# Performance work log

Measured on AMD Instinct MI355X. Metric: run time of the kernel, lower is better.

Reference implementation:

```python
import jax, jax.numpy as jnp
import numpy as np

N_GROUPS = 4
N_LIMITED_GROUPS = 2
TOP_K = 2
ROUTE_SCALE = 1.0


def setup_inputs() -> dict:
    key = jax.random.key(0)
    k1, k2, k3, k4 = jax.random.split(key, 4)
    n_tokens, dim, n_experts = 65536, 4096, 16
    return {
        "x": jax.random.normal(k1, (n_tokens, dim), dtype=jnp.float32),
        "w1_weight": jax.random.normal(k2, (n_experts, dim), dtype=jnp.float32) * 0.02,
        "w1_bias": jax.random.normal(k3, (n_experts,), dtype=jnp.float32) * 0.02,
        "route_bias": jax.random.normal(k4, (n_experts,), dtype=jnp.float32) * 0.02,
    }


def reference(x, w1_weight, w1_bias, route_bias):
    # Linear scorer: [N, E]
    logits = x @ w1_weight.T + w1_bias
    # softmax in fp32 (score_func == 'softmax')
    scores = jax.nn.softmax(logits.astype(jnp.float32), axis=-1)
    # bias add (moe_use_bias=True); original_scores includes the bias
    scores = scores + route_bias
    original_scores = scores

    n = x.shape[0]
    # group masking: view [N, n_groups, experts_per_group]
    g = scores.reshape(n, N_GROUPS, -1)
    group_scores = g.max(axis=-1)  # amax path since bias is not None
    _, gidx = jax.lax.top_k(group_scores, N_LIMITED_GROUPS)  # [N, n_limited]
    keep = jnp.zeros((n, N_GROUPS), dtype=bool).at[
        jnp.arange(n)[:, None], gidx
    ].set(True)
    masked = jnp.where(keep[:, :, None], g, -jnp.inf).reshape(n, -1)

    # top-k over masked scores; gather values from original (unmasked-at-topk) scores
    _, indices = jax.lax.top_k(masked, TOP_K)  # [N, k]
    values = jnp.take_along_axis(original_scores, indices, axis=1) * ROUTE_SCALE
    return values.astype(x.dtype), indices
```

## Files before the change

### kernel.cpp

```cpp
#include <hip/hip_runtime.h>
#include <math.h>

constexpr int NE  = 16;
constexpr int NG  = 4;
constexpr int NSL = 4;
constexpr int KS  = 16;
constexpr int TPB = 128;
constexpr int LDS_BYTES = 52224;

__global__ __launch_bounds__(256)
void w_transpose_kernel(const float* __restrict__ w, float* __restrict__ wt,
                        int dim, int n) {
    int id = blockIdx.x * 256 + threadIdx.x;
    if (id < n) {
        int k = id / NE;
        int e = id - k * NE;
        wt[id] = w[(size_t)e * dim + k];
    }
}

template <int WT>
__global__ __launch_bounds__(256)
void router_kernel(const float* __restrict__ x,
                   const float* __restrict__ w1w,
                   const float* __restrict__ wt,
                   const float* __restrict__ w1b,
                   const float* __restrict__ rbias,
                   float* __restrict__ dout,
                   int n_tokens, int dim)
{
    __shared__ char ldsraw[LDS_BYTES];
    auto wbuf = (double (*)[KS][NE])ldsraw;

    const int tid  = threadIdx.x;
    const int uwid = __builtin_amdgcn_readfirstlane(tid >> 6);
    const int lane = tid & 63;
    const int slice = dim / NSL;
    const int nst  = slice / KS;
    const long tokA = (long)blockIdx.x * TPB + lane;
    const long tokB = tokA + 64;

    const float* xA = x + tokA * (size_t)dim + (size_t)uwid * slice;
    const float* xB = x + tokB * (size_t)dim + (size_t)uwid * slice;

    double accA[NE], accB[NE];
#pragma unroll
    for (int e = 0; e < NE; ++e) { accA[e] = 0.0; accB[e] = 0.0; }

    float4 a0 = *(const float4*)(xA + 0),  a1 = *(const float4*)(xA + 4);
    float4 a2 = *(const float4*)(xA + 8),  a3 = *(const float4*)(xA + 12);
    float4 b0 = *(const float4*)(xB + 0),  b1 = *(const float4*)(xB + 4);
    float4 b2 = *(const float4*)(xB + 8),  b3 = *(const float4*)(xB + 12);

    float4 wreg;
    if (WT) {
        wreg = *(const float4*)(wt + (size_t)uwid * slice * NE + lane * 4);
    } else {
        const int i0 = lane * 4;
#pragma unroll
        for (int j = 0; j < 4; ++j) {
            int i = i0 + j;
            ((float*)&wreg)[j] = w1w[(size_t)(i & 15) * dim + uwid * slice + (i >> 4)];
        }
    }

    for (int c = 0; c < nst; ++c) {
        {
            double* dst = &wbuf[uwid][0][0] + lane * 4;
            dst[0] = (double)wreg.x;  dst[1] = (double)wreg.y;
            dst[2] = (double)wreg.z;  dst[3] = (double)wreg.w;
        }

        float4 na0 = a0, na1 = a1, na2 = a2, na3 = a3;
        float4 nb0 = b0, nb1 = b1, nb2 = b2, nb3 = b3;
        if (c + 1 < nst) {
            const float* pa = xA + (c + 1) * KS;
            const float* pb = xB + (c + 1) * KS;
            na0 = *(const float4*)(pa + 0);  na1 = *(const float4*)(pa + 4);
            na2 = *(const float4*)(pa + 8);  na3 = *(const float4*)(pa + 12);
            nb0 = *(const float4*)(pb + 0);  nb1 = *(const float4*)(pb + 4);
            nb2 = *(const float4*)(pb + 8);  nb3 = *(const float4*)(pb + 12);
            if (WT) {
                wreg = *(const float4*)(wt + (size_t)(uwid * slice + (c + 1) * KS) * NE
                                        + lane * 4);
            } else {
                const int kb = uwid * slice + (c + 1) * KS;
                const int i0 = lane * 4;
#pragma unroll
                for (int j = 0; j < 4; ++j) {
                    int i = i0 + j;
                    ((float*)&wreg)[j] = w1w[(size_t)(i & 15) * dim + kb + (i >> 4)];
                }
            }
        }

        float fa[KS], fb[KS];
        fa[0]=a0.x;  fa[1]=a0.y;  fa[2]=a0.z;  fa[3]=a0.w;
        fa[4]=a1.x;  fa[5]=a1.y;  fa[6]=a1.z;  fa[7]=a1.w;
        fa[8]=a2.x;  fa[9]=a2.y;  fa[10]=a2.z; fa[11]=a2.w;
        fa[12]=a3.x; fa[13]=a3.y; fa[14]=a3.z; fa[15]=a3.w;
        fb[0]=b0.x;  fb[1]=b0.y;  fb[2]=b0.z;  fb[3]=b0.w;
        fb[4]=b1.x;  fb[5]=b1.y;  fb[6]=b1.z;  fb[7]=b1.w;
        fb[8]=b2.x;  fb[9]=b2.y;  fb[10]=b2.z; fb[11]=b2.w;
        fb[12]=b3.x; fb[13]=b3.y; fb[14]=b3.z; fb[15]=b3.w;

#pragma unroll
        for (int kk = 0; kk < KS; ++kk) {
            double xa_ = (double)fa[kk];
            double xb_ = (double)fb[kk];
#pragma unroll
            for (int ep = 0; ep < NE / 2; ++ep) {
                double2 wv = *(const double2*)&wbuf[uwid][kk][ep * 2];
                accA[ep * 2 + 0] = fma(xa_, wv.x, accA[ep * 2 + 0]);
                accA[ep * 2 + 1] = fma(xa_, wv.y, accA[ep * 2 + 1]);
                accB[ep * 2 + 0] = fma(xb_, wv.x, accB[ep * 2 + 0]);
                accB[ep * 2 + 1] = fma(xb_, wv.y, accB[ep * 2 + 1]);
            }
        }

        a0=na0; a1=na1; a2=na2; a3=na3;
        b0=nb0; b1=nb1; b2=nb2; b3=nb3;
    }

    __syncthreads();
    auto red = (double (*)[2][64][NE + 1])ldsraw;
    if (uwid != 0) {
#pragma unroll
        for (int e = 0; e < NE; ++e) {
            red[uwid - 1][0][lane][e] = accA[e];
            red[uwid - 1][1][lane][e] = accB[e];
        }
    }
    __syncthreads();
    if (uwid != 0) return;

#pragma unroll
    for (int t = 0; t < 2; ++t) {
        double tot[NE];
#pragma unroll
        for (int e = 0; e < NE; ++e) {
            double a = (t == 0) ? accA[e] : accB[e];
            tot[e] = ((a + red[0][t][lane][e]) + red[1][t][lane][e])
                     + red[2][t][lane][e];
        }

        double logit[NE];
        double m = -INFINITY;
#pragma unroll
        for (int e = 0; e < NE; ++e) {
            logit[e] = tot[e] + (double)w1b[e];
            m = fmax(m, logit[e]);
        }
        double ssum = 0.0;
        double p[NE];
#pragma unroll
        for (int e = 0; e < NE; ++e) { p[e] = exp(logit[e] - m); ssum += p[e]; }
        double inv = 1.0 / ssum;
        double sc[NE];
#pragma unroll
        for (int e = 0; e < NE; ++e) sc[e] = p[e] * inv + (double)rbias[e];

        double gm[NG];
#pragma unroll
        for (int g = 0; g < NG; ++g) {
            double a = fmax(sc[g * 4 + 0], sc[g * 4 + 1]);
            double b = fmax(sc[g * 4 + 2], sc[g * 4 + 3]);
            gm[g] = fmax(a, b);
        }
        int g1 = 0;
#pragma unroll
        for (int g = 1; g < NG; ++g) if (gm[g] > gm[g1]) g1 = g;
        int g2 = (g1 == 0) ? 1 : 0;
#pragma unroll
        for (int g = 0; g < NG; ++g) if (g != g1 && gm[g] > gm[g2]) g2 = g;

        double v1 = -INFINITY; int i1 = 0;
#pragma unroll
        for (int e = 0; e < NE; ++e) {
            int g = e >> 2;
            bool keep = (g == g1) || (g == g2);
            if (keep && sc[e] > v1) { v1 = sc[e]; i1 = e; }
        }
        double v2 = -INFINITY; int i2 = 0;
#pragma unroll
        for (int e = 0; e < NE; ++e) {
            int g = e >> 2;
            bool keep = ((g == g1) || (g == g2)) && (e != i1);
            if (keep && sc[e] > v2) { v2 = sc[e]; i2 = e; }
        }

        long tok = (t == 0) ? tokA : tokB;
        float2 vv; vv.x = (float)v1; vv.y = (float)v2;
        *(float2*)(dout + tok * 2) = vv;
        float2 iv; iv.x = (float)i1; iv.y = (float)i2;
        *(float2*)(dout + (long)n_tokens * 2 + tok * 2) = iv;
    }
}

extern "C" void kernel_launch(void* const* d_in, const int* in_sizes, int n_in,
                              void* d_out, int out_size, void* d_ws, size_t ws_size,
                              hipStream_t stream)
{
    const float* x   = (const float*)d_in[0];
    const float* w1w = (const float*)d_in[1];
    const float* w1b = (const float*)d_in[2];
    const float* rb  = (const float*)d_in[3];
    float* out = (float*)d_out;

    const int ne       = in_sizes[2];
    const int dim      = in_sizes[1] / ne;
    const int n_tokens = in_sizes[0] / dim;

    const int nW = dim * ne;
    const bool useT = ws_size >= (size_t)nW * sizeof(float);

    dim3 grid(n_tokens / TPB), block(NSL * 64);
    if (useT) {
        float* wt = (float*)d_ws;
        hipLaunchKernelGGL(w_transpose_kernel, dim3((nW + 255) / 256), dim3(256),
                           0, stream, w1w, wt, dim, nW);
        hipLaunchKernelGGL((router_kernel<1>), grid, block, 0, stream,
                           x, w1w, (const float*)wt, w1b, rb, out, n_tokens, dim);
    } else {
        hipLaunchKernelGGL((router_kernel<0>), grid, block, 0, stream,
                           x, w1w, (const float*)nullptr, w1b, rb, out, n_tokens, dim);
    }
}
```

Baseline: 297.1 us.

## Split router into partial-sum kernel with 8 K-slices and separate finalize kernel

The fused router kernel is split into two kernels. The first computes fp64 partial dot products over 8 K-slices per 128-token block with a smaller LDS footprint, aiming for higher occupancy, and writes the partials to workspace. The second kernel reduces the partials and runs the softmax and top-k selection. This removes the in-block LDS reduction and barriers, but adds 64 MB of fp64 partial traffic to global memory and an extra kernel launch. If the workspace is too small, a fallback fused kernel runs instead.

```diff
diff --git a/kernel.cpp b/kernel.cpp
--- a/kernel.cpp
+++ b/kernel.cpp
@@ -3,10 +3,9 @@
 
 constexpr int NE  = 16;
 constexpr int NG  = 4;
-constexpr int NSL = 4;
-constexpr int KS  = 16;
-constexpr int TPB = 128;
-constexpr int LDS_BYTES = 52224;
+constexpr int NSL = 8;
+constexpr int KS  = 8;
+constexpr int TPB1 = 128;
 
 __global__ __launch_bounds__(256)
 void w_transpose_kernel(const float* __restrict__ w, float* __restrict__ wt,
@@ -19,90 +18,54 @@
     }
 }
 
-template <int WT>
-__global__ __launch_bounds__(256)
-void router_kernel(const float* __restrict__ x,
-                   const float* __restrict__ w1w,
-                   const float* __restrict__ wt,
-                   const float* __restrict__ w1b,
-                   const float* __restrict__ rbias,
-                   float* __restrict__ dout,
-                   int n_tokens, int dim)
+__global__ __launch_bounds__(512, 4)
+void k1_partials(const float* __restrict__ x,
+                 const float* __restrict__ wt,
+                 double* __restrict__ P,
+                 int n_tokens, int dim)
 {
-    __shared__ char ldsraw[LDS_BYTES];
-    auto wbuf = (double (*)[KS][NE])ldsraw;
+    __shared__ double wbuf[NSL][KS][NE];
 
     const int tid  = threadIdx.x;
     const int uwid = __builtin_amdgcn_readfirstlane(tid >> 6);
     const int lane = tid & 63;
     const int slice = dim / NSL;
     const int nst  = slice / KS;
-    const long tokA = (long)blockIdx.x * TPB + lane;
+    const long tokA = (long)blockIdx.x * TPB1 + lane;
     const long tokB = tokA + 64;
 
     const float* xA = x + tokA * (size_t)dim + (size_t)uwid * slice;
     const float* xB = x + tokB * (size_t)dim + (size_t)uwid * slice;
+    const float* wp = wt + (size_t)uwid * slice * NE;
 
     double accA[NE], accB[NE];
 #pragma unroll
     for (int e = 0; e < NE; ++e) { accA[e] = 0.0; accB[e] = 0.0; }
 
-    float4 a0 = *(const float4*)(xA + 0),  a1 = *(const float4*)(xA + 4);
-    float4 a2 = *(const float4*)(xA + 8),  a3 = *(const float4*)(xA + 12);
-    float4 b0 = *(const float4*)(xB + 0),  b1 = *(const float4*)(xB + 4);
-    float4 b2 = *(const float4*)(xB + 8),  b3 = *(const float4*)(xB + 12);
-
-    float4 wreg;
-    if (WT) {
-        wreg = *(const float4*)(wt + (size_t)uwid * slice * NE + lane * 4);
-    } else {
-        const int i0 = lane * 4;
-#pragma unroll
-        for (int j = 0; j < 4; ++j) {
-            int i = i0 + j;
-            ((float*)&wreg)[j] = w1w[(size_t)(i & 15) * dim + uwid * slice + (i >> 4)];
-        }
-    }
+    float4 a0 = *(const float4*)(xA + 0), a1 = *(const float4*)(xA + 4);
+    float4 b0 = *(const float4*)(xB + 0), b1 = *(const float4*)(xB + 4);
+    float2 wreg = *(const float2*)(wp + lane * 2);
 
     for (int c = 0; c < nst; ++c) {
         {
-            double* dst = &wbuf[uwid][0][0] + lane * 4;
+            double* dst = &wbuf[uwid][0][0] + lane * 2;
             dst[0] = (double)wreg.x;  dst[1] = (double)wreg.y;
-            dst[2] = (double)wreg.z;  dst[3] = (double)wreg.w;
-        }
-
-        float4 na0 = a0, na1 = a1, na2 = a2, na3 = a3;
-        float4 nb0 = b0, nb1 = b1, nb2 = b2, nb3 = b3;
+        }
+
+        float4 na0 = a0, na1 = a1, nb0 = b0, nb1 = b1;
         if (c + 1 < nst) {
             const float* pa = xA + (c + 1) * KS;
             const float* pb = xB + (c + 1) * KS;
             na0 = *(const float4*)(pa + 0);  na1 = *(const float4*)(pa + 4);
-            na2 = *(const float4*)(pa + 8);  na3 = *(const float4*)(pa + 12);
             nb0 = *(const float4*)(pb + 0);  nb1 = *(const float4*)(pb + 4);
-            nb2 = *(const float4*)(pb + 8);  nb3 = *(const float4*)(pb + 12);
-            if (WT) {
-                wreg = *(const float4*)(wt + (size_t)(uwid * slice + (c + 1) * KS) * NE
-                                        + lane * 4);
-            } else {
-                const int kb = uwid * slice + (c + 1) * KS;
-                const int i0 = lane * 4;
-#pragma unroll
-                for (int j = 0; j < 4; ++j) {
-                    int i = i0 + j;
-                    ((float*)&wreg)[j] = w1w[(size_t)(i & 15) * dim + kb + (i >> 4)];
-                }
-            }
+            wreg = *(const float2*)(wp + (size_t)(c + 1) * KS * NE + lane * 2);
         }
 
         float fa[KS], fb[KS];
-        fa[0]=a0.x;  fa[1]=a0.y;  fa[2]=a0.z;  fa[3]=a0.w;
-        fa[4]=a1.x;  fa[5]=a1.y;  fa[6]=a1.z;  fa[7]=a1.w;
-        fa[8]=a2.x;  fa[9]=a2.y;  fa[10]=a2.z; fa[11]=a2.w;
-        fa[12]=a3.x; fa[13]=a3.y; fa[14]=a3.z; fa[15]=a3.w;
-        fb[0]=b0.x;  fb[1]=b0.y;  fb[2]=b0.z;  fb[3]=b0.w;
-        fb[4]=b1.x;  fb[5]=b1.y;  fb[6]=b1.z;  fb[7]=b1.w;
-        fb[8]=b2.x;  fb[9]=b2.y;  fb[10]=b2.z; fb[11]=b2.w;
-        fb[12]=b3.x; fb[13]=b3.y; fb[14]=b3.z; fb[15]=b3.w;
+        fa[0]=a0.x; fa[1]=a0.y; fa[2]=a0.z; fa[3]=a0.w;
+        fa[4]=a1.x; fa[5]=a1.y; fa[6]=a1.z; fa[7]=a1.w;
+        fb[0]=b0.x; fb[1]=b0.y; fb[2]=b0.z; fb[3]=b0.w;
+        fb[4]=b1.x; fb[5]=b1.y; fb[6]=b1.z; fb[7]=b1.w;
 
 #pragma unroll
         for (int kk = 0; kk < KS; ++kk) {
@@ -118,12 +81,184 @@
             }
         }
 
+        a0 = na0; a1 = na1; b0 = nb0; b1 = nb1;
+    }
+
+    double* pA = P + ((size_t)uwid * n_tokens + tokA) * NE;
+    double* pB = P + ((size_t)uwid * n_tokens + tokB) * NE;
+#pragma unroll
+    for (int j = 0; j < NE / 2; ++j) {
+        double2 v; v.x = accA[2 * j]; v.y = accA[2 * j + 1];
+        *(double2*)(pA + 2 * j) = v;
+    }
+#pragma unroll
+    for (int j = 0; j < NE / 2; ++j) {
+        double2 v; v.x = accB[2 * j]; v.y = accB[2 * j + 1];
+        *(double2*)(pB + 2 * j) = v;
+    }
+}
+
+__global__ __launch_bounds__(256)
+void k2_finalize(const double* __restrict__ P,
+                 const float* __restrict__ w1b,
+                 const float* __restrict__ rbias,
+                 float* __restrict__ dout,
+                 int n_tokens)
+{
+    const long t = (long)blockIdx.x * 256 + threadIdx.x;
+    if (t >= n_tokens) return;
+
+    double tot[NE];
+#pragma unroll
+    for (int e = 0; e < NE; ++e) tot[e] = 0.0;
+    for (int s = 0; s < NSL; ++s) {
+        const double* ps = P + ((size_t)s * n_tokens + t) * NE;
+#pragma unroll
+        for (int j = 0; j < NE / 2; ++j) {
+            double2 v = *(const double2*)(ps + 2 * j);
+            tot[2 * j + 0] += v.x;
+            tot[2 * j + 1] += v.y;
+        }
+    }
+
+    double logit[NE];
+    double m = -INFINITY;
+#pragma unroll
+    for (int e = 0; e < NE; ++e) {
+        logit[e] = tot[e] + (double)w1b[e];
+        m = fmax(m, logit[e]);
+    }
+    double ssum = 0.0;
+    double p[NE];
+#pragma unroll
+    for (int e = 0; e < NE; ++e) { p[e] = exp(logit[e] - m); ssum += p[e]; }
+    double inv = 1.0 / ssum;
+    double sc[NE];
+#pragma unroll
+    for (int e = 0; e < NE; ++e) sc[e] = p[e] * inv + (double)rbias[e];
+
+    double gm[NG];
+#pragma unroll
+    for (int g = 0; g < NG; ++g) {
+        double a = fmax(sc[g * 4 + 0], sc[g * 4 + 1]);
+        double b = fmax(sc[g * 4 + 2], sc[g * 4 + 3]);
+        gm[g] = fmax(a, b);
+    }
+    int g1 = 0;
+#pragma unroll
+    for (int g = 1; g < NG; ++g) if (gm[g] > gm[g1]) g1 = g;
+    int g2 = (g1 == 0) ? 1 : 0;
+#pragma unroll
+    for (int g = 0; g < NG; ++g) if (g != g1 && gm[g] > gm[g2]) g2 = g;
+
+    double v1 = -INFINITY; int i1 = 0;
+#pragma unroll
+    for (int e = 0; e < NE; ++e) {
+        int g = e >> 2;
+        bool keep = (g == g1) || (g == g2);
+        if (keep && sc[e] > v1) { v1 = sc[e]; i1 = e; }
+    }
+    double v2 = -INFINITY; int i2 = 0;
+#pragma unroll
+    for (int e = 0; e < NE; ++e) {
+        int g = e >> 2;
+        bool keep = ((g == g1) || (g == g2)) && (e != i1);
+        if (keep && sc[e] > v2) { v2 = sc[e]; i2 = e; }
+    }
+
+    float2 vv; vv.x = (float)v1; vv.y = (float)v2;
+    *(float2*)(dout + t * 2) = vv;
+    float2 iv; iv.x = (float)i1; iv.y = (float)i2;
+    *(float2*)(dout + (long)n_tokens * 2 + t * 2) = iv;
+}
+
+__global__ __launch_bounds__(256)
+void router_fallback(const float* __restrict__ x,
+                     const float* __restrict__ w1w,
+                     const float* __restrict__ w1b,
+                     const float* __restrict__ rbias,
+                     float* __restrict__ dout,
+                     int n_tokens, int dim)
+{
+    __shared__ double wbuf4[4][16][NE];
+    const int tid  = threadIdx.x;
+    const int uwid = __builtin_amdgcn_readfirstlane(tid >> 6);
+    const int lane = tid & 63;
+    const int slice = dim / 4;
+    const int nst  = slice / 16;
+    const long tokA = (long)blockIdx.x * 128 + lane;
+    const long tokB = tokA + 64;
+    const float* xA = x + tokA * (size_t)dim + (size_t)uwid * slice;
+    const float* xB = x + tokB * (size_t)dim + (size_t)uwid * slice;
+
+    double accA[NE], accB[NE];
+#pragma unroll
+    for (int e = 0; e < NE; ++e) { accA[e] = 0.0; accB[e] = 0.0; }
+
+    float4 a0 = *(const float4*)(xA + 0), a1 = *(const float4*)(xA + 4);
+    float4 a2 = *(const float4*)(xA + 8), a3 = *(const float4*)(xA + 12);
+    float4 b0 = *(const float4*)(xB + 0), b1 = *(const float4*)(xB + 4);
+    float4 b2 = *(const float4*)(xB + 8), b3 = *(const float4*)(xB + 12);
+    float4 wreg;
+    {
+        const int i0 = lane * 4;
+#pragma unroll
+        for (int j = 0; j < 4; ++j) {
+            int i = i0 + j;
+            ((float*)&wreg)[j] = w1w[(size_t)(i & 15) * dim + uwid * slice + (i >> 4)];
+        }
+    }
+
+    for (int c = 0; c < nst; ++c) {
+        {
+            double* dst = &wbuf4[uwid][0][0] + lane * 4;
+            dst[0] = (double)wreg.x;  dst[1] = (double)wreg.y;
+            dst[2] = (double)wreg.z;  dst[3] = (double)wreg.w;
+        }
+        float4 na0=a0,na1=a1,na2=a2,na3=a3,nb0=b0,nb1=b1,nb2=b2,nb3=b3;
+        if (c + 1 < nst) {
+            const float* pa = xA + (c + 1) * 16;
+            const float* pb = xB + (c + 1) * 16;
+            na0 = *(const float4*)(pa + 0);  na1 = *(const float4*)(pa + 4);
+            na2 = *(const float4*)(pa + 8);  na3 = *(const float4*)(pa + 12);
+            nb0 = *(const float4*)(pb + 0);  nb1 = *(const float4*)(pb + 4);
+            nb2 = *(const float4*)(pb + 8);  nb3 = *(const float4*)(pb + 12);
+            const int kb = uwid * slice + (c + 1) * 16;
+            const int i0 = lane * 4;
+#pragma unroll
+            for (int j = 0; j < 4; ++j) {
+                int i = i0 + j;
+                ((float*)&wreg)[j] = w1w[(size_t)(i & 15) * dim + kb + (i >> 4)];
+            }
+        }
+        float fa[16], fb[16];
+        fa[0]=a0.x; fa[1]=a0.y; fa[2]=a0.z; fa[3]=a0.w;
+        fa[4]=a1.x; fa[5]=a1.y; fa[6]=a1.z; fa[7]=a1.w;
+        fa[8]=a2.x; fa[9]=a2.y; fa[10]=a2.z; fa[11]=a2.w;
+        fa[12]=a3.x; fa[13]=a3.y; fa[14]=a3.z; fa[15]=a3.w;
+        fb[0]=b0.x; fb[1]=b0.y; fb[2]=b0.z; fb[3]=b0.w;
+        fb[4]=b1.x; fb[5]=b1.y; fb[6]=b1.z; fb[7]=b1.w;
+        fb[8]=b2.x; fb[9]=b2.y; fb[10]=b2.z; fb[11]=b2.w;
+        fb[12]=b3.x; fb[13]=b3.y; fb[14]=b3.z; fb[15]=b3.w;
+#pragma unroll
+        for (int kk = 0; kk < 16; ++kk) {
+            double xa_ = (double)fa[kk];
+            double xb_ = (double)fb[kk];
+#pragma unroll
+            for (int ep = 0; ep < NE / 2; ++ep) {
+                double2 wv = *(const double2*)&wbuf4[uwid][kk][ep * 2];
+                accA[ep*2+0] = fma(xa_, wv.x, accA[ep*2+0]);
+                accA[ep*2+1] = fma(xa_, wv.y, accA[ep*2+1]);
+                accB[ep*2+0] = fma(xb_, wv.x, accB[ep*2+0]);
+                accB[ep*2+1] = fma(xb_, wv.y, accB[ep*2+1]);
+            }
+        }
         a0=na0; a1=na1; a2=na2; a3=na3;
         b0=nb0; b1=nb1; b2=nb2; b3=nb3;
     }
 
     __syncthreads();
-    auto red = (double (*)[2][64][NE + 1])ldsraw;
+    __shared__ double red[3][2][64][NE + 1];
     if (uwid != 0) {
 #pragma unroll
         for (int e = 0; e < NE; ++e) {
@@ -143,7 +278,6 @@
             tot[e] = ((a + red[0][t][lane][e]) + red[1][t][lane][e])
                      + red[2][t][lane][e];
         }
-
         double logit[NE];
         double m = -INFINITY;
 #pragma unroll
@@ -151,20 +285,17 @@
             logit[e] = tot[e] + (double)w1b[e];
             m = fmax(m, logit[e]);
         }
-        double ssum = 0.0;
-        double p[NE];
+        double ssum = 0.0, p[NE];
 #pragma unroll
         for (int e = 0; e < NE; ++e) { p[e] = exp(logit[e] - m); ssum += p[e]; }
-        double inv = 1.0 / ssum;
-        double sc[NE];
+        double inv = 1.0 / ssum, sc[NE];
 #pragma unroll
         for (int e = 0; e < NE; ++e) sc[e] = p[e] * inv + (double)rbias[e];
-
         double gm[NG];
 #pragma unroll
         for (int g = 0; g < NG; ++g) {
-            double a = fmax(sc[g * 4 + 0], sc[g * 4 + 1]);
-            double b = fmax(sc[g * 4 + 2], sc[g * 4 + 3]);
+            double a = fmax(sc[g*4+0], sc[g*4+1]);
+            double b = fmax(sc[g*4+2], sc[g*4+3]);
             gm[g] = fmax(a, b);
         }
         int g1 = 0;
@@ -173,7 +304,6 @@
         int g2 = (g1 == 0) ? 1 : 0;
 #pragma unroll
         for (int g = 0; g < NG; ++g) if (g != g1 && gm[g] > gm[g2]) g2 = g;
-
         double v1 = -INFINITY; int i1 = 0;
 #pragma unroll
         for (int e = 0; e < NE; ++e) {
@@ -188,7 +318,6 @@
             bool keep = ((g == g1) || (g == g2)) && (e != i1);
             if (keep && sc[e] > v2) { v2 = sc[e]; i2 = e; }
         }
-
         long tok = (t == 0) ? tokA : tokB;
         float2 vv; vv.x = (float)v1; vv.y = (float)v2;
         *(float2*)(dout + tok * 2) = vv;
@@ -212,17 +341,20 @@
     const int n_tokens = in_sizes[0] / dim;
 
     const int nW = dim * ne;
-    const bool useT = ws_size >= (size_t)nW * sizeof(float);
-
-    dim3 grid(n_tokens / TPB), block(NSL * 64);
-    if (useT) {
-        float* wt = (float*)d_ws;
+    const size_t partials_bytes = (size_t)NSL * n_tokens * NE * sizeof(double);
+    const size_t need = partials_bytes + (size_t)nW * sizeof(float);
+
+    if (ws_size >= need) {
+        double* P  = (double*)d_ws;
+        float*  wt = (float*)((char*)d_ws + partials_bytes);
         hipLaunchKernelGGL(w_transpose_kernel, dim3((nW + 255) / 256), dim3(256),
                            0, stream, w1w, wt, dim, nW);
-        hipLaunchKernelGGL((router_kernel<1>), grid, block, 0, stream,
-                           x, w1w, (const float*)wt, w1b, rb, out, n_tokens, dim);
+        hipLaunchKernelGGL(k1_partials, dim3(n_tokens / TPB1), dim3(NSL * 64),
+                           0, stream, x, wt, P, n_tokens, dim);
+        hipLaunchKernelGGL(k2_finalize, dim3((n_tokens + 255) / 256), dim3(256),
+                           0, stream, P, w1b, rb, out, n_tokens);
     } else {
-        hipLaunchKernelGGL((router_kernel<0>), grid, block, 0, stream,
-                           x, w1w, (const float*)nullptr, w1b, rb, out, n_tokens, dim);
-    }
-}
+        hipLaunchKernelGGL(router_fallback, dim3(n_tokens / 128), dim3(256),
+                           0, stream, x, w1w, w1b, rb, out, n_tokens, dim);
+    }
+}
```

Result: slower. 502.1 us (+69.0%).
